# Optimization experiments

Measured on AMD Instinct MI355X. Metric: run time of the kernel, lower is better.

The kernel has to match this reference:

```python
import jax, jax.numpy as jnp
import numpy as np

WIN_SIZE = 11
SIGMA = 1.5
DATA_RANGE = 1.0
K1, K2 = 0.01, 0.03


def _gaussian_1d(size=WIN_SIZE, sigma=SIGMA):
    coords = np.arange(size, dtype=np.float32) - (size - 1) / 2.0
    g = np.exp(-(coords ** 2) / (2.0 * sigma ** 2))
    g = g / g.sum()
    return jnp.asarray(g, dtype=jnp.float32)


def _gaussian_blur(x):
    # Separable depthwise Gaussian blur, VALID padding (matches pytorch-msssim).
    B, C, H, W = x.shape
    g = _gaussian_1d().astype(x.dtype)
    kh = jnp.tile(g.reshape(1, 1, WIN_SIZE, 1), (C, 1, 1, 1))
    kw = jnp.tile(g.reshape(1, 1, 1, WIN_SIZE), (C, 1, 1, 1))
    dn = ('NCHW', 'OIHW', 'NCHW')
    x = jax.lax.conv_general_dilated(x, kh, (1, 1), 'VALID',
                                     dimension_numbers=dn, feature_group_count=C)
    x = jax.lax.conv_general_dilated(x, kw, (1, 1), 'VALID',
                                     dimension_numbers=dn, feature_group_count=C)
    return x


def _ssim(X, Y):
    C1 = (K1 * DATA_RANGE) ** 2
    C2 = (K2 * DATA_RANGE) ** 2

    mu1 = _gaussian_blur(X)
    mu2 = _gaussian_blur(Y)
    mu1_sq = mu1 * mu1
    mu2_sq = mu2 * mu2
    mu1_mu2 = mu1 * mu2

    sigma1_sq = _gaussian_blur(X * X) - mu1_sq
    sigma2_sq = _gaussian_blur(Y * Y) - mu2_sq
    sigma12 = _gaussian_blur(X * Y) - mu1_mu2

    cs_map = (2.0 * sigma12 + C2) / (sigma1_sq + sigma2_sq + C2)
    ssim_map = ((2.0 * mu1_mu2 + C1) / (mu1_sq + mu2_sq + C1)) * cs_map

    ssim_per_channel = ssim_map.mean(axis=(2, 3))  # [B, C]
    return ssim_per_channel


def setup_inputs() -> dict:
    key = jax.random.key(0)
    k1, k2 = jax.random.split(key)
    predictions = jax.random.uniform(k1, (32, 3, 512, 512), dtype=jnp.float32)
    labels = jax.random.uniform(k2, (32, 3, 512, 512), dtype=jnp.float32)
    return {"predictions": predictions, "labels": labels}


def reference(predictions, labels):
    ssim_per_channel = _ssim(predictions, labels)
    # nonnegative_ssim=True -> relu; size_average=True -> scalar mean
    ssim_val = jax.nn.relu(ssim_per_channel).mean()
    return 1.0 - ssim_val
```

## Files before the change

kernel.cpp:

```cpp
#include <hip/hip_runtime.h>


#define TW 32
#define TH 32
#define IH 42
#define WIN 11
#define OUT_DIM 502
#define IMG 512
#define NPLANES 96

__device__ __forceinline__ float4 ldg4(const float* p) { return *(const float4*)p; }

__global__ __launch_bounds__(256, 4) void ssim_tile(const float* __restrict__ X,
                                                    const float* __restrict__ Y,
                                                    float* __restrict__ planeSums) {
    constexpr float G[WIN] = {0.00102838f, 0.00759875f, 0.03600077f, 0.10936071f,
                              0.21300553f, 0.26601172f, 0.21300553f, 0.10936071f,
                              0.03600077f, 0.00759875f, 0.00102838f};

    __shared__ float sH[5][IH][TW];

    const int tid = threadIdx.x;
    const int ox = blockIdx.x * TW;
    const int oy = blockIdx.y * TH;
    const int plane = blockIdx.z;
    const float* Xp = X + (size_t)plane * IMG * IMG;
    const float* Yp = Y + (size_t)plane * IMG * IMG;

    for (int s = tid; s < IH * (TW / 4); s += 256) {
        const int r = s >> 3;
        const int j0 = (s & 7) << 2;
        const int gr = oy + r;
        float x[16], y[16];
        if (gr < IMG) {
            const float* px = Xp + gr * IMG + ox + j0;
            const float* py = Yp + gr * IMG + ox + j0;
            if (ox + j0 + 16 <= IMG) {
                #pragma unroll
                for (int q = 0; q < 4; ++q) {
                    *(float4*)&x[q * 4] = ldg4(px + q * 4);
                    *(float4*)&y[q * 4] = ldg4(py + q * 4);
                }
            } else {
                #pragma unroll
                for (int q = 0; q < 16; ++q) {
                    const int gc = ox + j0 + q;
                    x[q] = (gc < IMG) ? px[q] : 0.f;
                    y[q] = (gc < IMG) ? py[q] : 0.f;
                }
            }
        } else {
            #pragma unroll
            for (int q = 0; q < 16; ++q) { x[q] = 0.f; y[q] = 0.f; }
        }
        float h0[4] = {0,0,0,0}, h1[4] = {0,0,0,0}, h2[4] = {0,0,0,0},
              h3[4] = {0,0,0,0}, h4[4] = {0,0,0,0};
        #pragma unroll
        for (int k = 0; k < WIN; ++k) {
            const float w = G[k];
            #pragma unroll
            for (int c = 0; c < 4; ++c) {
                const float xv = x[k + c], yv = y[k + c];
                const float wx = w * xv, wy = w * yv;
                h0[c] += wx;
                h1[c] += wy;
                h2[c] += wx * xv;
                h3[c] += wy * yv;
                h4[c] += wx * yv;
            }
        }
        *(float4*)&sH[0][r][j0] = *(float4*)h0;
        *(float4*)&sH[1][r][j0] = *(float4*)h1;
        *(float4*)&sH[2][r][j0] = *(float4*)h2;
        *(float4*)&sH[3][r][j0] = *(float4*)h3;
        *(float4*)&sH[4][r][j0] = *(float4*)h4;
    }
    __syncthreads();

    const int j = tid & 31;
    const int i0 = (tid >> 5) << 2;
    float mu1[4] = {0,0,0,0}, mu2[4] = {0,0,0,0};
    float vxx[4] = {0,0,0,0}, vyy[4] = {0,0,0,0}, vxy[4] = {0,0,0,0};
    #pragma unroll
    for (int k = 0; k < 14; ++k) {
        const float v0 = sH[0][i0 + k][j];
        const float v1 = sH[1][i0 + k][j];
        const float v2 = sH[2][i0 + k][j];
        const float v3 = sH[3][i0 + k][j];
        const float v4 = sH[4][i0 + k][j];
        #pragma unroll
        for (int i = 0; i < 4; ++i) {
            const int kk = k - i;
            if (kk >= 0 && kk < WIN) {
                const float w = G[kk];
                mu1[i] += w * v0;
                mu2[i] += w * v1;
                vxx[i] += w * v2;
                vyy[i] += w * v3;
                vxy[i] += w * v4;
            }
        }
    }

    const float C1 = 0.0001f;
    const float C2 = 0.0009f;
    float local = 0.f;
    #pragma unroll
    for (int i = 0; i < 4; ++i) {
        if ((oy + i0 + i) < OUT_DIM && (ox + j) < OUT_DIM) {
            const float m1 = mu1[i], m2 = mu2[i];
            const float m1sq = m1 * m1, m2sq = m2 * m2, m12 = m1 * m2;
            const float s1  = vxx[i] - m1sq;
            const float s2  = vyy[i] - m2sq;
            const float s12 = vxy[i] - m12;
            const float num = (2.f * m12 + C1) * (2.f * s12 + C2);
            const float den = (m1sq + m2sq + C1) * (s1 + s2 + C2);
            local += num * __builtin_amdgcn_rcpf(den);
        }
    }

    #pragma unroll
    for (int off = 32; off > 0; off >>= 1)
        local += __shfl_down(local, off, 64);
    __shared__ float red[4];
    const int wave = tid >> 6;
    const int lane = tid & 63;
    if (lane == 0) red[wave] = local;
    __syncthreads();
    if (tid == 0) {
        const float s = (red[0] + red[1]) + (red[2] + red[3]);
        atomicAdd(&planeSums[plane], s);
    }
}

__global__ __launch_bounds__(128) void ssim_finalize(const float* __restrict__ planeSums,
                                                     float* __restrict__ out) {
    const int tid = threadIdx.x;
    float v = 0.f;
    if (tid < NPLANES) {
        const float m = planeSums[tid] * (1.0f / (float)(OUT_DIM * OUT_DIM));
        v = fmaxf(m, 0.f);
    }
    #pragma unroll
    for (int off = 32; off > 0; off >>= 1)
        v += __shfl_down(v, off, 64);
    __shared__ float red[2];
    if ((tid & 63) == 0) red[tid >> 6] = v;
    __syncthreads();
    if (tid == 0) out[0] = 1.0f - (red[0] + red[1]) * (1.0f / (float)NPLANES);
}

extern "C" void kernel_launch(void* const* d_in, const int* in_sizes, int n_in,
                              void* d_out, int out_size, void* d_ws, size_t ws_size,
                              hipStream_t stream) {
    const float* X = (const float*)d_in[0];
    const float* Y = (const float*)d_in[1];
    float* out = (float*)d_out;
    float* ws  = (float*)d_ws;

    hipMemsetAsync(ws, 0, NPLANES * sizeof(float), stream);

    dim3 grid(IMG / TW, IMG / TH, NPLANES);
    ssim_tile<<<grid, 256, 0, stream>>>(X, Y, ws);
    ssim_finalize<<<1, 128, 0, stream>>>(ws, out);
}
```

Baseline: 370.0 us.

## Stream row bands with register ring buffer for vertical Gaussian pass

Replaces 32x32 tiles, which recompute a 10-row halo and stage horizontal results in shared memory, with full-width 64-row bands per block. Each thread owns two columns, computes the horizontal blur from a 4-row shared ring buffer, and accumulates the vertical blur into an 11-deep register ring of partial sums. This removes most halo recomputation and the shared-memory round trip of the five blurred maps. In exchange it uses many more registers (110 accumulators), needs a barrier per row, and launches far fewer blocks (768), which lowers parallelism and occupancy.

```diff
diff --git a/kernel.cpp b/kernel.cpp
--- a/kernel.cpp
+++ b/kernel.cpp
@@ -1,121 +1,130 @@
 #include <hip/hip_runtime.h>
 
 
-#define TW 32
-#define TH 32
-#define IH 42
+#define IMG 512
+#define OUT_DIM 502
 #define WIN 11
-#define OUT_DIM 502
-#define IMG 512
+#define BH 64
 #define NPLANES 96
+#define LW 524
 
-__device__ __forceinline__ float4 ldg4(const float* p) { return *(const float4*)p; }
-
-__global__ __launch_bounds__(256, 4) void ssim_tile(const float* __restrict__ X,
-                                                    const float* __restrict__ Y,
-                                                    float* __restrict__ planeSums) {
+__global__ __launch_bounds__(256, 3) void ssim_stream(const float* __restrict__ X,
+                                                      const float* __restrict__ Y,
+                                                      float* __restrict__ planeSums) {
     constexpr float G[WIN] = {0.00102838f, 0.00759875f, 0.03600077f, 0.10936071f,
                               0.21300553f, 0.26601172f, 0.21300553f, 0.10936071f,
                               0.03600077f, 0.00759875f, 0.00102838f};
 
-    __shared__ float sH[5][IH][TW];
+    __shared__ float xs[4][LW];
+    __shared__ float ys[4][LW];
 
     const int tid = threadIdx.x;
-    const int ox = blockIdx.x * TW;
-    const int oy = blockIdx.y * TH;
-    const int plane = blockIdx.z;
-    const float* Xp = X + (size_t)plane * IMG * IMG;
-    const float* Yp = Y + (size_t)plane * IMG * IMG;
+    const int band = blockIdx.x;
+    const int plane = blockIdx.y;
+    const int r0 = band * BH;
+    const size_t pbase = (size_t)plane * IMG * IMG;
+    const float* Xp = X + pbase;
+    const float* Yp = Y + pbase;
+    const int c0 = tid << 1;
+    const int validEnd = min(r0 + BH, OUT_DIM);
 
-    for (int s = tid; s < IH * (TW / 4); s += 256) {
-        const int r = s >> 3;
-        const int j0 = (s & 7) << 2;
-        const int gr = oy + r;
-        float x[16], y[16];
-        if (gr < IMG) {
-            const float* px = Xp + gr * IMG + ox + j0;
-            const float* py = Yp + gr * IMG + ox + j0;
-            if (ox + j0 + 16 <= IMG) {
+    if (tid < 48) {
+        const int slot = tid / 12, p = tid - slot * 12;
+        xs[slot][IMG + p] = 0.f;
+        ys[slot][IMG + p] = 0.f;
+    }
+    #pragma unroll
+    for (int i = 0; i < 2; ++i) {
+        const float2 xv = *(const float2*)(Xp + (r0 + i) * IMG + c0);
+        const float2 yv = *(const float2*)(Yp + (r0 + i) * IMG + c0);
+        *(float2*)&xs[i][c0] = xv;
+        *(float2*)&ys[i][c0] = yv;
+    }
+    __syncthreads();
+
+    float a[5][2][WIN];
+    float local = 0.f;
+
+    for (int base = 0; base < 77; base += WIN) {
+        #pragma unroll
+        for (int ph = 0; ph < WIN; ++ph) {
+            const int p = base + ph;
+            const int r = r0 + p;
+
+            float2 px = make_float2(0.f, 0.f), py = make_float2(0.f, 0.f);
+            const int rp = r + 2;
+            if (rp < IMG) {
+                px = *(const float2*)(Xp + rp * IMG + c0);
+                py = *(const float2*)(Yp + rp * IMG + c0);
+            }
+
+            float h[5][2];
+            if (r < IMG) {
+                float xr[12], yr[12];
+                const float* xrow = xs[p & 3];
+                const float* yrow = ys[p & 3];
                 #pragma unroll
-                for (int q = 0; q < 4; ++q) {
-                    *(float4*)&x[q * 4] = ldg4(px + q * 4);
-                    *(float4*)&y[q * 4] = ldg4(py + q * 4);
+                for (int i = 0; i < 6; ++i) {
+                    *(float2*)&xr[2 * i] = *(const float2*)&xrow[c0 + 2 * i];
+                    *(float2*)&yr[2 * i] = *(const float2*)&yrow[c0 + 2 * i];
+                }
+                #pragma unroll
+                for (int c = 0; c < 2; ++c) {
+                    float h0 = 0.f, h1 = 0.f, h2 = 0.f, h3 = 0.f, h4 = 0.f;
+                    #pragma unroll
+                    for (int k = 0; k < WIN; ++k) {
+                        const float w = G[k];
+                        const float xv = xr[k + c], yv = yr[k + c];
+                        const float wx = w * xv, wy = w * yv;
+                        h0 += wx;
+                        h1 += wy;
+                        h2 = fmaf(wx, xv, h2);
+                        h3 = fmaf(wy, yv, h3);
+                        h4 = fmaf(wx, yv, h4);
+                    }
+                    h[0][c] = h0; h[1][c] = h1; h[2][c] = h2; h[3][c] = h3; h[4][c] = h4;
                 }
             } else {
                 #pragma unroll
-                for (int q = 0; q < 16; ++q) {
-                    const int gc = ox + j0 + q;
-                    x[q] = (gc < IMG) ? px[q] : 0.f;
-                    y[q] = (gc < IMG) ? py[q] : 0.f;
+                for (int m = 0; m < 5; ++m) { h[m][0] = 0.f; h[m][1] = 0.f; }
+            }
+
+            #pragma unroll
+            for (int d = 0; d < WIN; ++d) {
+                const int s = (ph - d + 22) % WIN;
+                const float w = G[d];
+                #pragma unroll
+                for (int m = 0; m < 5; ++m) {
+                    #pragma unroll
+                    for (int c = 0; c < 2; ++c) {
+                        if (d == 0) a[m][c][s] = w * h[m][c];
+                        else        a[m][c][s] = fmaf(w, h[m][c], a[m][c][s]);
+                    }
                 }
             }
-        } else {
-            #pragma unroll
-            for (int q = 0; q < 16; ++q) { x[q] = 0.f; y[q] = 0.f; }
-        }
-        float h0[4] = {0,0,0,0}, h1[4] = {0,0,0,0}, h2[4] = {0,0,0,0},
-              h3[4] = {0,0,0,0}, h4[4] = {0,0,0,0};
-        #pragma unroll
-        for (int k = 0; k < WIN; ++k) {
-            const float w = G[k];
-            #pragma unroll
-            for (int c = 0; c < 4; ++c) {
-                const float xv = x[k + c], yv = y[k + c];
-                const float wx = w * xv, wy = w * yv;
-                h0[c] += wx;
-                h1[c] += wy;
-                h2[c] += wx * xv;
-                h3[c] += wy * yv;
-                h4[c] += wx * yv;
+
+            const int o = r0 + p - 10;
+            if (p >= 10 && o < validEnd) {
+                const int se = (ph + 1) % WIN;
+                const float C1 = 0.0001f, C2 = 0.0009f;
+                #pragma unroll
+                for (int c = 0; c < 2; ++c) {
+                    if (c0 + c < OUT_DIM) {
+                        const float m1 = a[0][c][se], m2 = a[1][c][se];
+                        const float m1sq = m1 * m1, m2sq = m2 * m2, m12 = m1 * m2;
+                        const float s1  = a[2][c][se] - m1sq;
+                        const float s2  = a[3][c][se] - m2sq;
+                        const float s12 = a[4][c][se] - m12;
+                        const float num = (2.f * m12 + C1) * (2.f * s12 + C2);
+                        const float den = (m1sq + m2sq + C1) * (s1 + s2 + C2);
+                        local += num * __builtin_amdgcn_rcpf(den);
+                    }
+                }
             }
-        }
-        *(float4*)&sH[0][r][j0] = *(float4*)h0;
-        *(float4*)&sH[1][r][j0] = *(float4*)h1;
-        *(float4*)&sH[2][r][j0] = *(float4*)h2;
-        *(float4*)&sH[3][r][j0] = *(float4*)h3;
-        *(float4*)&sH[4][r][j0] = *(float4*)h4;
-    }
-    __syncthreads();
 
-    const int j = tid & 31;
-    const int i0 = (tid >> 5) << 2;
-    float mu1[4] = {0,0,0,0}, mu2[4] = {0,0,0,0};
-    float vxx[4] = {0,0,0,0}, vyy[4] = {0,0,0,0}, vxy[4] = {0,0,0,0};
-    #pragma unroll
-    for (int k = 0; k < 14; ++k) {
-        const float v0 = sH[0][i0 + k][j];
-        const float v1 = sH[1][i0 + k][j];
-        const float v2 = sH[2][i0 + k][j];
-        const float v3 = sH[3][i0 + k][j];
-        const float v4 = sH[4][i0 + k][j];
-        #pragma unroll
-        for (int i = 0; i < 4; ++i) {
-            const int kk = k - i;
-            if (kk >= 0 && kk < WIN) {
-                const float w = G[kk];
-                mu1[i] += w * v0;
-                mu2[i] += w * v1;
-                vxx[i] += w * v2;
-                vyy[i] += w * v3;
-                vxy[i] += w * v4;
-            }
-        }
-    }
-
-    const float C1 = 0.0001f;
-    const float C2 = 0.0009f;
-    float local = 0.f;
-    #pragma unroll
-    for (int i = 0; i < 4; ++i) {
-        if ((oy + i0 + i) < OUT_DIM && (ox + j) < OUT_DIM) {
-            const float m1 = mu1[i], m2 = mu2[i];
-            const float m1sq = m1 * m1, m2sq = m2 * m2, m12 = m1 * m2;
-            const float s1  = vxx[i] - m1sq;
-            const float s2  = vyy[i] - m2sq;
-            const float s12 = vxy[i] - m12;
-            const float num = (2.f * m12 + C1) * (2.f * s12 + C2);
-            const float den = (m1sq + m2sq + C1) * (s1 + s2 + C2);
-            local += num * __builtin_amdgcn_rcpf(den);
+            __syncthreads();
+            *(float2*)&xs[(p + 2) & 3][c0] = px;
+            *(float2*)&ys[(p + 2) & 3][c0] = py;
         }
     }
 
@@ -123,14 +132,10 @@
     for (int off = 32; off > 0; off >>= 1)
         local += __shfl_down(local, off, 64);
     __shared__ float red[4];
-    const int wave = tid >> 6;
-    const int lane = tid & 63;
-    if (lane == 0) red[wave] = local;
+    if ((tid & 63) == 0) red[tid >> 6] = local;
     __syncthreads();
-    if (tid == 0) {
-        const float s = (red[0] + red[1]) + (red[2] + red[3]);
-        atomicAdd(&planeSums[plane], s);
-    }
+    if (tid == 0)
+        atomicAdd(&planeSums[plane], (red[0] + red[1]) + (red[2] + red[3]));
 }
 
 __global__ __launch_bounds__(128) void ssim_finalize(const float* __restrict__ planeSums,
@@ -160,7 +165,7 @@
 
     hipMemsetAsync(ws, 0, NPLANES * sizeof(float), stream);
 
-    dim3 grid(IMG / TW, IMG / TH, NPLANES);
-    ssim_tile<<<grid, 256, 0, stream>>>(X, Y, ws);
+    dim3 grid(IMG / BH, NPLANES);
+    ssim_stream<<<grid, 256, 0, stream>>>(X, Y, ws);
     ssim_finalize<<<1, 128, 0, stream>>>(ws, out);
 }
```

New measurement: 770.8 us. 108% more time.
